# Optimization experiments

Measured on AMD Instinct MI355X. Metric: run time of the kernel, lower is better.

Reference implementation:

```python
import jax, jax.numpy as jnp
import numpy as np

N_MIN = 5
N_MAX = 16
VARIANTS_PER_N = 16
NUM_HIDDEN = 2
HIDDEN = 512
TOTAL_MODELS = (N_MAX - N_MIN + 1) * VARIANTS_PER_N  # 192
BATCH = 65536


def setup_inputs() -> dict:
    key = jax.random.key(0)
    ks = jax.random.split(key, 8)
    n = 16
    s_in = 1.0 / np.sqrt(n)
    s_h = 1.0 / np.sqrt(HIDDEN)
    return {
        "T": jax.random.normal(ks[0], (BATCH, n), dtype=jnp.float32),
        "n": n,
        "variant_index": 3,
        "w_in": jax.random.normal(ks[1], (TOTAL_MODELS, HIDDEN, N_MAX), dtype=jnp.float32) * s_in,
        "b_in": jax.random.normal(ks[2], (TOTAL_MODELS, HIDDEN), dtype=jnp.float32) * 0.01,
        "w_hid": jax.random.normal(ks[3], (TOTAL_MODELS, NUM_HIDDEN, HIDDEN, HIDDEN), dtype=jnp.float32) * s_h,
        "b_hid": jax.random.normal(ks[4], (TOTAL_MODELS, NUM_HIDDEN, HIDDEN), dtype=jnp.float32) * 0.01,
        "w_out": jax.random.normal(ks[5], (TOTAL_MODELS, N_MAX + 1, HIDDEN), dtype=jnp.float32) * s_h,
        "b_out": jax.random.normal(ks[6], (TOTAL_MODELS, N_MAX + 1), dtype=jnp.float32) * 0.01,
    }


def _distortion(X, n):
    # X: (B, n+1). Z[:, n-1-i] = sum_j X[:, j] * X[:, j+i+1] (zero-padded shift).
    # lag k = i+1 -> column n-k; loop is over fixed small n (<=16), unrolls statically.
    cols = [jnp.sum(X[:, :-k] * X[:, k:], axis=1) for k in range(1, n + 1)]
    return jnp.stack(cols[::-1], axis=1)  # (B, n)


def reference(T, n, variant_index, w_in, b_in, w_hid, b_hid, w_out, b_out):
    model_idx = (n - N_MIN) * VARIANTS_PER_N + variant_index
    wi = w_in[model_idx]    # (H, N_MAX)
    bi = b_in[model_idx]    # (H,)
    wh = w_hid[model_idx]   # (2, H, H)
    bh = b_hid[model_idx]   # (2, H)
    wo = w_out[model_idx]   # (N_MAX+1, H)
    bo = b_out[model_idx]   # (N_MAX+1,)

    T_pad = jnp.pad(T, ((0, 0), (0, N_MAX - n)))  # (B, N_MAX)
    norm = jnp.sqrt(jnp.clip(jnp.sum(T_pad * T_pad, axis=1, keepdims=True), 1e-12))
    T_unit = T_pad / norm
    scale = jnp.sqrt(norm)

    x = jax.nn.silu(T_unit @ wi.T + bi)
    for h in range(NUM_HIDDEN):
        x = jax.nn.relu(x @ wh[h].T + bh[h])
    x_full = (x @ wo.T + bo) * scale  # (B, N_MAX+1)

    X_hat = x_full[:, :n + 1]
    X_hat_clamped = jnp.clip(X_hat, -2.0, 2.0)
    error = jnp.mean((_distortion(X_hat, n) - T) ** 2)
    error_clamped = jnp.mean((_distortion(X_hat_clamped, n) - T) ** 2)
    return (X_hat, error, X_hat_clamped, error_clamped)
```

## Files before the change

kernel.cpp:

```cpp
#include <hip/hip_runtime.h>

#define BATCH 65536
#define MT 128
#define NBLK (BATCH / MT)

typedef unsigned short u16;
typedef __bf16 bf16x8 __attribute__((ext_vector_type(8)));
typedef float f32x4 __attribute__((ext_vector_type(4)));

#define WI_OFF 0
#define WH_OFF 16384
#define WO_OFF 540672
#define WS_USH 557056
#define BI_F 0
#define BH_F 512
#define BO_F 1536
#define PART_F 1568
#define PREP_WH 65536
#define PREP_WI 2048
#define PREP_WO 2048
#define PREP_SC 1568
#define PREP_TOTAL (PREP_WH + PREP_WI + PREP_WO + PREP_SC)

__device__ inline u16 f2bf(float f) {
  union { float f; unsigned u; } v; v.f = f;
  unsigned u = v.u + 0x7fffu + ((v.u >> 16) & 1u);
  return (u16)(u >> 16);
}

__global__ void prep_kernel(const float* __restrict__ w_in, const float* __restrict__ b_in,
                            const float* __restrict__ w_hid, const float* __restrict__ b_hid,
                            const float* __restrict__ w_out, const float* __restrict__ b_out,
                            const int* __restrict__ variant, int n,
                            u16* __restrict__ wsu, float* __restrict__ wsf)
{
  const int model = (n - 5) * 16 + variant[0];
  const int i = blockIdx.x * 256 + threadIdx.x;
  if (i < PREP_WH) {
    int g = i & 3, col = (i >> 2) & 511, K32 = (i >> 11) & 15, l = i >> 15;
    const float* src = w_hid + (size_t)model * 524288 + (size_t)l * 262144 + col * 512 + K32 * 32 + g * 8;
    u16* dst = wsu + WH_OFF + (size_t)i * 8;
    #pragma unroll
    for (int e = 0; e < 8; ++e) dst[e] = f2bf(src[e]);
  } else if (i < PREP_WH + PREP_WI) {
    int j = i - PREP_WH;
    int g = j & 3, col = j >> 2;
    u16* dst = wsu + WI_OFF + (size_t)j * 8;
    #pragma unroll
    for (int e = 0; e < 8; ++e) {
      int k = g * 8 + e;
      dst[e] = (k < 16) ? f2bf(w_in[(size_t)model * 8192 + col * 16 + k]) : (u16)0;
    }
  } else if (i < PREP_WH + PREP_WI + PREP_WO) {
    int j = i - PREP_WH - PREP_WI;
    int g = j & 3, col = (j >> 2) & 31, K32 = j >> 7;
    u16* dst = wsu + WO_OFF + (size_t)j * 8;
    #pragma unroll
    for (int e = 0; e < 8; ++e) {
      int k = K32 * 32 + g * 8 + e;
      dst[e] = (col < 17) ? f2bf(w_out[(size_t)model * 8704 + col * 512 + k]) : (u16)0;
    }
  } else if (i < PREP_TOTAL) {
    int j = i - PREP_WH - PREP_WI - PREP_WO;
    if (j < 512)       wsf[BI_F + j] = b_in[(size_t)model * 512 + j];
    else if (j < 1536) wsf[BH_F + (j - 512)] = b_hid[(size_t)model * 1024 + (j - 512)];
    else               { int o = j - 1536; wsf[BO_F + o] = (o < 17) ? b_out[(size_t)model * 17 + o] : 0.f; }
  }
}

__device__ __forceinline__ bf16x8 rdA(const char* xb, int row, int kbyte) {
  return *reinterpret_cast<const bf16x8*>(xb + row * 1024 + (kbyte ^ ((row & 15) << 4)));
}
__device__ __forceinline__ void st16(char* xb, int row, int col, u16 v) {
  *(u16*)(xb + row * 1024 + ((col * 2) ^ ((row & 15) << 4))) = v;
}

template<int NK>
__device__ __forceinline__ void dense_layer(const u16* __restrict__ Wp,
                                            const float* __restrict__ bias, int act,
                                            char* xb, int l15, int q, int c0, int koff)
{
  f32x4 acc[2][4][4];
  #pragma unroll
  for (int p = 0; p < 2; ++p)
    #pragma unroll
    for (int a = 0; a < 4; ++a)
      #pragma unroll
      for (int b = 0; b < 4; ++b) { f32x4 z = {0.f, 0.f, 0.f, 0.f}; acc[p][a][b] = z; }

  const u16* Wl = Wp + (c0 + l15) * 32 + q * 8;

  if constexpr (NK == 1) {
    uint4 b0[4];
    #pragma unroll
    for (int ct = 0; ct < 4; ++ct)
      b0[ct] = *reinterpret_cast<const uint4*>(Wl + ct * 512);
    const int kb = q * 16;
    #pragma unroll
    for (int p = 0; p < 2; ++p)
      #pragma unroll
      for (int mt = 0; mt < 4; ++mt) {
        bf16x8 a = rdA(xb, p * 64 + mt * 16 + l15, kb);
        #pragma unroll
        for (int ct = 0; ct < 4; ++ct)
          acc[p][mt][ct] = __builtin_amdgcn_mfma_f32_16x16x32_bf16(
              a, __builtin_bit_cast(bf16x8, b0[ct]), acc[p][mt][ct], 0, 0, 0);
      }
  } else {
    uint4 bc[4], bn[4];
    {
      const u16* p = Wl + (size_t)koff * 16384;
      #pragma unroll
      for (int ct = 0; ct < 4; ++ct)
        bc[ct] = *reinterpret_cast<const uint4*>(p + ct * 512);
    }
    #pragma unroll 1
    for (int i = 0; i < NK; i += 2) {
      {
        const int Kb = (i + 1) ^ koff;
        const u16* p = Wl + (size_t)Kb * 16384;
        #pragma unroll
        for (int ct = 0; ct < 4; ++ct)
          bn[ct] = *reinterpret_cast<const uint4*>(p + ct * 512);
      }
      {
        const int kb = ((i ^ koff) * 64) + q * 16;
        #pragma unroll
        for (int p = 0; p < 2; ++p)
          #pragma unroll
          for (int mt = 0; mt < 4; ++mt) {
            bf16x8 a = rdA(xb, p * 64 + mt * 16 + l15, kb);
            #pragma unroll
            for (int ct = 0; ct < 4; ++ct)
              acc[p][mt][ct] = __builtin_amdgcn_mfma_f32_16x16x32_bf16(
                  a, __builtin_bit_cast(bf16x8, bc[ct]), acc[p][mt][ct], 0, 0, 0);
          }
      }
      {
        const int Kc = ((i + 2) & (NK - 1)) ^ koff;
        const u16* p = Wl + (size_t)Kc * 16384;
        #pragma unroll
        for (int ct = 0; ct < 4; ++ct)
          bc[ct] = *reinterpret_cast<const uint4*>(p + ct * 512);
      }
      {
        const int kb = (((i + 1) ^ koff) * 64) + q * 16;
        #pragma unroll
        for (int p = 0; p < 2; ++p)
          #pragma unroll
          for (int mt = 0; mt < 4; ++mt) {
            bf16x8 a = rdA(xb, p * 64 + mt * 16 + l15, kb);
            #pragma unroll
            for (int ct = 0; ct < 4; ++ct)
              acc[p][mt][ct] = __builtin_amdgcn_mfma_f32_16x16x32_bf16(
                  a, __builtin_bit_cast(bf16x8, bn[ct]), acc[p][mt][ct], 0, 0, 0);
          }
      }
    }
  }
  __syncthreads();

  float bv[4];
  #pragma unroll
  for (int ct = 0; ct < 4; ++ct) bv[ct] = bias[c0 + ct * 16 + l15];
  #pragma unroll
  for (int p = 0; p < 2; ++p)
    #pragma unroll
    for (int mt = 0; mt < 4; ++mt)
      #pragma unroll
      for (int ct = 0; ct < 4; ++ct)
        #pragma unroll
        for (int j = 0; j < 4; ++j) {
          int row = p * 64 + mt * 16 + q * 4 + j;
          float z = acc[p][mt][ct][j] + bv[ct];
          float h = act ? fmaxf(z, 0.f) : z / (1.f + __expf(-z));
          st16(xb, row, c0 + ct * 16 + l15, f2bf(h));
        }
  __syncthreads();
}

template<int CN>
__global__ __launch_bounds__(512, 2) void fused_kernel(
    const float* __restrict__ T, const u16* __restrict__ wsu,
    const float* __restrict__ wsf, float* __restrict__ Xout, float* __restrict__ Xcout,
    float* __restrict__ errPart, int n_arg)
{
  const int n = CN ? CN : n_arg;
  __shared__ u16 xs[MT * 512];
  __shared__ float xo[MT * 20];
  __shared__ float scaleS[MT];
  __shared__ float ered[8][2];

  const int tid = threadIdx.x;
  const int blk = blockIdx.x;
  const int lane = tid & 63;
  const int wid = tid >> 6;
  const int l15 = lane & 15;
  const int q = lane >> 4;
  const int c0 = wid * 64;
  const int koff = (blk >> 3) & 15;
  char* xb = (char*)xs;

  {
    const int r = tid >> 2, j = tid & 3;
    const size_t gr = (size_t)blk * MT + r;
    const float* tp = T + gr * n;
    float v[4]; float ss = 0.f;
    #pragma unroll
    for (int c = 0; c < 4; ++c) {
      int k = j * 4 + c;
      v[c] = (k < n) ? tp[k] : 0.f;
      ss += v[c] * v[c];
    }
    ss += __shfl_xor(ss, 1); ss += __shfl_xor(ss, 2);
    float norm = sqrtf(ss < 1e-12f ? 1e-12f : ss);
    float rn = 1.f / norm;
    if (j == 0) scaleS[r] = sqrtf(norm);
    #pragma unroll
    for (int c = 0; c < 4; ++c) {
      st16(xb, r, j * 4 + c, f2bf(v[c] * rn));
      st16(xb, r, 16 + j * 4 + c, 0);
    }
  }
  __syncthreads();

  dense_layer<1 >(wsu + WI_OFF,          wsf + BI_F,       0, xb, l15, q, c0, 0);
  dense_layer<16>(wsu + WH_OFF,          wsf + BH_F,       1, xb, l15, q, c0, koff);
  dense_layer<16>(wsu + WH_OFF + 262144, wsf + BH_F + 512, 1, xb, l15, q, c0, koff);

  {
    f32x4 oacc[2];
    { f32x4 z = {0.f, 0.f, 0.f, 0.f}; oacc[0] = z; oacc[1] = z; }
    const int bofs2 = l15 * 32 + q * 8;
    uint4 ob[2], on[2];
    #pragma unroll
    for (int ct = 0; ct < 2; ++ct)
      ob[ct] = *reinterpret_cast<const uint4*>(wsu + WO_OFF + bofs2 + ct * 512);
    #pragma unroll
    for (int K2 = 0; K2 < 16; K2 += 2) {
      #pragma unroll
      for (int ct = 0; ct < 2; ++ct)
        on[ct] = *reinterpret_cast<const uint4*>(wsu + WO_OFF + (K2 + 1) * 1024 + bofs2 + ct * 512);
      {
        bf16x8 a = rdA(xb, wid * 16 + l15, K2 * 64 + q * 16);
        #pragma unroll
        for (int ct = 0; ct < 2; ++ct)
          oacc[ct] = __builtin_amdgcn_mfma_f32_16x16x32_bf16(
              a, __builtin_bit_cast(bf16x8, ob[ct]), oacc[ct], 0, 0, 0);
      }
      if (K2 + 2 < 16) {
        #pragma unroll
        for (int ct = 0; ct < 2; ++ct)
          ob[ct] = *reinterpret_cast<const uint4*>(wsu + WO_OFF + (K2 + 2) * 1024 + bofs2 + ct * 512);
      }
      {
        bf16x8 a = rdA(xb, wid * 16 + l15, (K2 + 1) * 64 + q * 16);
        #pragma unroll
        for (int ct = 0; ct < 2; ++ct)
          oacc[ct] = __builtin_amdgcn_mfma_f32_16x16x32_bf16(
              a, __builtin_bit_cast(bf16x8, on[ct]), oacc[ct], 0, 0, 0);
      }
    }
    #pragma unroll
    for (int ct = 0; ct < 2; ++ct)
      #pragma unroll
      for (int j = 0; j < 4; ++j) {
        int o = ct * 16 + l15;
        int row = wid * 16 + q * 4 + j;
        if (o <= n) {
          float val = (oacc[ct][j] + wsf[BO_F + o]) * scaleS[row];
          size_t gr = (size_t)blk * MT + row;
          float cv = fminf(fmaxf(val, -2.f), 2.f);
          Xout[gr * (n + 1) + o] = val;
          Xcout[gr * (n + 1) + o] = cv;
          xo[row * 20 + o] = val;
        }
      }
  }
  __syncthreads();

  {
    const int r = tid >> 2, j = tid & 3;
    const size_t gr = (size_t)blk * MT + r;
    float x[17], cx[17];
    #pragma unroll
    for (int i = 0; i < 17; ++i) {
      float v = (i <= n) ? xo[r * 20 + i] : 0.f;
      x[i] = v; cx[i] = fminf(fmaxf(v, -2.f), 2.f);
    }
    float e = 0.f, ec = 0.f;
    #pragma unroll
    for (int kk = 0; kk < 4; ++kk) {
      int k = j + 1 + kk * 4;
      if (k <= n) {
        float d = 0.f, dc = 0.f;
        #pragma unroll
        for (int i = 0; i < 16; ++i) {
          if (i + k <= 16) {
            if (i + k <= n) { d += x[i] * x[i + k]; dc += cx[i] * cx[i + k]; }
          }
        }
        float tvv = T[gr * n + (n - k)];
        float r1 = d - tvv, r2 = dc - tvv;
        e += r1 * r1; ec += r2 * r2;
      }
    }
    e += __shfl_xor(e, 1);  ec += __shfl_xor(ec, 1);
    e += __shfl_xor(e, 2);  ec += __shfl_xor(ec, 2);
    e += __shfl_xor(e, 4);  ec += __shfl_xor(ec, 4);
    e += __shfl_xor(e, 8);  ec += __shfl_xor(ec, 8);
    e += __shfl_xor(e, 16); ec += __shfl_xor(ec, 16);
    e += __shfl_xor(e, 32); ec += __shfl_xor(ec, 32);
    if (lane == 0) { ered[wid][0] = e; ered[wid][1] = ec; }
  }
  __syncthreads();
  if (tid == 0) {
    float e = 0.f, ec = 0.f;
    #pragma unroll
    for (int w = 0; w < 8; ++w) { e += ered[w][0]; ec += ered[w][1]; }
    errPart[blk * 2]     = e;
    errPart[blk * 2 + 1] = ec;
  }
}

__global__ void finalize_kernel(const float* __restrict__ part, float* __restrict__ e0,
                                float* __restrict__ e1, float inv)
{
  __shared__ float se[4][2];
  const int t = threadIdx.x;
  float e = 0.f, ec = 0.f;
  for (int b = t; b < NBLK; b += 256) { e += part[2 * b]; ec += part[2 * b + 1]; }
  e += __shfl_xor(e, 1);  ec += __shfl_xor(ec, 1);
  e += __shfl_xor(e, 2);  ec += __shfl_xor(ec, 2);
  e += __shfl_xor(e, 4);  ec += __shfl_xor(ec, 4);
  e += __shfl_xor(e, 8);  ec += __shfl_xor(ec, 8);
  e += __shfl_xor(e, 16); ec += __shfl_xor(ec, 16);
  e += __shfl_xor(e, 32); ec += __shfl_xor(ec, 32);
  if ((t & 63) == 0) { se[t >> 6][0] = e; se[t >> 6][1] = ec; }
  __syncthreads();
  if (t == 0) {
    float te = 0.f, tec = 0.f;
    #pragma unroll
    for (int w = 0; w < 4; ++w) { te += se[w][0]; tec += se[w][1]; }
    e0[0] = te * inv;
    e1[0] = tec * inv;
  }
}

extern "C" void kernel_launch(void* const* d_in, const int* in_sizes, int n_in,
                              void* d_out, int out_size, void* d_ws, size_t ws_size,
                              hipStream_t stream)
{
  const float* T       = (const float*)d_in[0];
  const int*   variant = (const int*)d_in[2];
  const float* w_in    = (const float*)d_in[3];
  const float* b_in    = (const float*)d_in[4];
  const float* w_hid   = (const float*)d_in[5];
  const float* b_hid   = (const float*)d_in[6];
  const float* w_out   = (const float*)d_in[7];
  const float* b_out   = (const float*)d_in[8];
  const int n = in_sizes[0] / BATCH;

  u16* wsu = (u16*)d_ws;
  float* wsf = (float*)((char*)d_ws + (size_t)WS_USH * 2);
  float* out = (float*)d_out;
  const size_t xe = (size_t)BATCH * (n + 1);
  float* Xo  = out;
  float* eP  = out + xe;
  float* Xc  = out + xe + 1;
  float* ecP = out + 2 * xe + 1;

  const int prepBlocks = (PREP_TOTAL + 255) / 256;
  prep_kernel<<<prepBlocks, 256, 0, stream>>>(w_in, b_in, w_hid, b_hid, w_out, b_out,
                                              variant, n, wsu, wsf);
  if (n == 16)
    fused_kernel<16><<<NBLK, 512, 0, stream>>>(T, wsu, wsf, Xo, Xc, wsf + PART_F, n);
  else
    fused_kernel<0><<<NBLK, 512, 0, stream>>>(T, wsu, wsf, Xo, Xc, wsf + PART_F, n);
  finalize_kernel<<<1, 256, 0, stream>>>(wsf + PART_F, eP, ecP, 1.f / (float)((size_t)BATCH * n));
}
```

Before: 135.6 us.

## Triple-buffer weight loads, prefetch next layer weights, cache T in LDS

Replaces the double-buffered, rolled K loop (which used a per-block koff rotation to stagger weight reads) with a fully unrolled triple-buffered prefetch of weight fragments. The first fragment of each next layer's weights is loaded before the barrier and activation epilogue, so that latency overlaps the epilogue. s_setprio is raised around the MFMA sections, and T is staged in LDS so the error pass does not re-read it from global memory. The cost is more VGPRs under the 512x2 launch bound, a larger unrolled code body, and dropping koff, which may concentrate L2 traffic on the same weight lines across blocks.

Measured after the change: 236.3 us. 74.2% more time.

```diff
diff --git a/kernel.cpp b/kernel.cpp
--- a/kernel.cpp
+++ b/kernel.cpp
@@ -77,8 +77,10 @@
 
 template<int NK>
 __device__ __forceinline__ void dense_layer(const u16* __restrict__ Wp,
+                                            const u16* __restrict__ Wnext,
                                             const float* __restrict__ bias, int act,
-                                            char* xb, int l15, int q, int c0, int koff)
+                                            char* xb, int l15, int q, int c0,
+                                            uint4 (&pre)[4])
 {
   f32x4 acc[2][4][4];
   #pragma unroll
@@ -90,12 +92,25 @@
 
   const u16* Wl = Wp + (c0 + l15) * 32 + q * 8;
 
-  if constexpr (NK == 1) {
-    uint4 b0[4];
+  uint4 buf[3][4];
+  #pragma unroll
+  for (int ct = 0; ct < 4; ++ct) buf[0][ct] = pre[ct];
+  if constexpr (NK > 1) {
     #pragma unroll
     for (int ct = 0; ct < 4; ++ct)
-      b0[ct] = *reinterpret_cast<const uint4*>(Wl + ct * 512);
-    const int kb = q * 16;
+      buf[1][ct] = *reinterpret_cast<const uint4*>(Wl + 16384 + ct * 512);
+  }
+
+  #pragma unroll
+  for (int i = 0; i < NK; ++i) {
+    if (i + 2 < NK) {
+      #pragma unroll
+      for (int ct = 0; ct < 4; ++ct)
+        buf[(i + 2) % 3][ct] =
+            *reinterpret_cast<const uint4*>(Wl + (size_t)(i + 2) * 16384 + ct * 512);
+    }
+    __builtin_amdgcn_s_setprio(1);
+    const int kb = i * 64 + q * 16;
     #pragma unroll
     for (int p = 0; p < 2; ++p)
       #pragma unroll
@@ -104,59 +119,16 @@
         #pragma unroll
         for (int ct = 0; ct < 4; ++ct)
           acc[p][mt][ct] = __builtin_amdgcn_mfma_f32_16x16x32_bf16(
-              a, __builtin_bit_cast(bf16x8, b0[ct]), acc[p][mt][ct], 0, 0, 0);
+              a, __builtin_bit_cast(bf16x8, buf[i % 3][ct]), acc[p][mt][ct], 0, 0, 0);
       }
-  } else {
-    uint4 bc[4], bn[4];
-    {
-      const u16* p = Wl + (size_t)koff * 16384;
-      #pragma unroll
-      for (int ct = 0; ct < 4; ++ct)
-        bc[ct] = *reinterpret_cast<const uint4*>(p + ct * 512);
-    }
-    #pragma unroll 1
-    for (int i = 0; i < NK; i += 2) {
-      {
-        const int Kb = (i + 1) ^ koff;
-        const u16* p = Wl + (size_t)Kb * 16384;
-        #pragma unroll
-        for (int ct = 0; ct < 4; ++ct)
-          bn[ct] = *reinterpret_cast<const uint4*>(p + ct * 512);
-      }
-      {
-        const int kb = ((i ^ koff) * 64) + q * 16;
-        #pragma unroll
-        for (int p = 0; p < 2; ++p)
-          #pragma unroll
-          for (int mt = 0; mt < 4; ++mt) {
-            bf16x8 a = rdA(xb, p * 64 + mt * 16 + l15, kb);
-            #pragma unroll
-            for (int ct = 0; ct < 4; ++ct)
-              acc[p][mt][ct] = __builtin_amdgcn_mfma_f32_16x16x32_bf16(
-                  a, __builtin_bit_cast(bf16x8, bc[ct]), acc[p][mt][ct], 0, 0, 0);
-          }
-      }
-      {
-        const int Kc = ((i + 2) & (NK - 1)) ^ koff;
-        const u16* p = Wl + (size_t)Kc * 16384;
-        #pragma unroll
-        for (int ct = 0; ct < 4; ++ct)
-          bc[ct] = *reinterpret_cast<const uint4*>(p + ct * 512);
-      }
-      {
-        const int kb = (((i + 1) ^ koff) * 64) + q * 16;
-        #pragma unroll
-        for (int p = 0; p < 2; ++p)
-          #pragma unroll
-          for (int mt = 0; mt < 4; ++mt) {
-            bf16x8 a = rdA(xb, p * 64 + mt * 16 + l15, kb);
-            #pragma unroll
-            for (int ct = 0; ct < 4; ++ct)
-              acc[p][mt][ct] = __builtin_amdgcn_mfma_f32_16x16x32_bf16(
-                  a, __builtin_bit_cast(bf16x8, bn[ct]), acc[p][mt][ct], 0, 0, 0);
-          }
-      }
-    }
+    __builtin_amdgcn_s_setprio(0);
+  }
+
+  if (Wnext != nullptr) {
+    const u16* Wn = Wnext + (c0 + l15) * 32 + q * 8;
+    #pragma unroll
+    for (int ct = 0; ct < 4; ++ct)
+      pre[ct] = *reinterpret_cast<const uint4*>(Wn + ct * 512);
   }
   __syncthreads();
 
@@ -188,6 +160,7 @@
   const int n = CN ? CN : n_arg;
   __shared__ u16 xs[MT * 512];
   __shared__ float xo[MT * 20];
+  __shared__ float ts[MT * 16];
   __shared__ float scaleS[MT];
   __shared__ float ered[8][2];
 
@@ -198,8 +171,15 @@
   const int l15 = lane & 15;
   const int q = lane >> 4;
   const int c0 = wid * 64;
-  const int koff = (blk >> 3) & 15;
   char* xb = (char*)xs;
+
+  uint4 pre[4];
+  {
+    const u16* WiL = wsu + WI_OFF + (c0 + l15) * 32 + q * 8;
+    #pragma unroll
+    for (int ct = 0; ct < 4; ++ct)
+      pre[ct] = *reinterpret_cast<const uint4*>(WiL + ct * 512);
+  }
 
   {
     const int r = tid >> 2, j = tid & 3;
@@ -220,46 +200,40 @@
     for (int c = 0; c < 4; ++c) {
       st16(xb, r, j * 4 + c, f2bf(v[c] * rn));
       st16(xb, r, 16 + j * 4 + c, 0);
-    }
-  }
-  __syncthreads();
-
-  dense_layer<1 >(wsu + WI_OFF,          wsf + BI_F,       0, xb, l15, q, c0, 0);
-  dense_layer<16>(wsu + WH_OFF,          wsf + BH_F,       1, xb, l15, q, c0, koff);
-  dense_layer<16>(wsu + WH_OFF + 262144, wsf + BH_F + 512, 1, xb, l15, q, c0, koff);
+      ts[r * 16 + j * 4 + c] = v[c];
+    }
+  }
+  __syncthreads();
+
+  dense_layer<1 >(wsu + WI_OFF, wsu + WH_OFF, wsf + BI_F, 0, xb, l15, q, c0, pre);
+  dense_layer<16>(wsu + WH_OFF, wsu + WH_OFF + 262144, wsf + BH_F, 1, xb, l15, q, c0, pre);
+  dense_layer<16>(wsu + WH_OFF + 262144, nullptr, wsf + BH_F + 512, 1, xb, l15, q, c0, pre);
 
   {
     f32x4 oacc[2];
     { f32x4 z = {0.f, 0.f, 0.f, 0.f}; oacc[0] = z; oacc[1] = z; }
     const int bofs2 = l15 * 32 + q * 8;
-    uint4 ob[2], on[2];
-    #pragma unroll
-    for (int ct = 0; ct < 2; ++ct)
-      ob[ct] = *reinterpret_cast<const uint4*>(wsu + WO_OFF + bofs2 + ct * 512);
-    #pragma unroll
-    for (int K2 = 0; K2 < 16; K2 += 2) {
+    uint4 ob[3][2];
+    #pragma unroll
+    for (int s = 0; s < 2; ++s)
       #pragma unroll
       for (int ct = 0; ct < 2; ++ct)
-        on[ct] = *reinterpret_cast<const uint4*>(wsu + WO_OFF + (K2 + 1) * 1024 + bofs2 + ct * 512);
-      {
-        bf16x8 a = rdA(xb, wid * 16 + l15, K2 * 64 + q * 16);
+        ob[s][ct] = *reinterpret_cast<const uint4*>(wsu + WO_OFF + s * 1024 + bofs2 + ct * 512);
+    #pragma unroll
+    for (int K = 0; K < 16; ++K) {
+      if (K + 2 < 16) {
         #pragma unroll
         for (int ct = 0; ct < 2; ++ct)
-          oacc[ct] = __builtin_amdgcn_mfma_f32_16x16x32_bf16(
-              a, __builtin_bit_cast(bf16x8, ob[ct]), oacc[ct], 0, 0, 0);
+          ob[(K + 2) % 3][ct] =
+              *reinterpret_cast<const uint4*>(wsu + WO_OFF + (K + 2) * 1024 + bofs2 + ct * 512);
       }
-      if (K2 + 2 < 16) {
-        #pragma unroll
-        for (int ct = 0; ct < 2; ++ct)
-          ob[ct] = *reinterpret_cast<const uint4*>(wsu + WO_OFF + (K2 + 2) * 1024 + bofs2 + ct * 512);
-      }
-      {
-        bf16x8 a = rdA(xb, wid * 16 + l15, (K2 + 1) * 64 + q * 16);
-        #pragma unroll
-        for (int ct = 0; ct < 2; ++ct)
-          oacc[ct] = __builtin_amdgcn_mfma_f32_16x16x32_bf16(
-              a, __builtin_bit_cast(bf16x8, on[ct]), oacc[ct], 0, 0, 0);
-      }
+      __builtin_amdgcn_s_setprio(1);
+      bf16x8 a = rdA(xb, wid * 16 + l15, K * 64 + q * 16);
+      #pragma unroll
+      for (int ct = 0; ct < 2; ++ct)
+        oacc[ct] = __builtin_amdgcn_mfma_f32_16x16x32_bf16(
+            a, __builtin_bit_cast(bf16x8, ob[K % 3][ct]), oacc[ct], 0, 0, 0);
+      __builtin_amdgcn_s_setprio(0);
     }
     #pragma unroll
     for (int ct = 0; ct < 2; ++ct)
@@ -281,7 +255,6 @@
 
   {
     const int r = tid >> 2, j = tid & 3;
-    const size_t gr = (size_t)blk * MT + r;
     float x[17], cx[17];
     #pragma unroll
     for (int i = 0; i < 17; ++i) {
@@ -300,7 +273,7 @@
             if (i + k <= n) { d += x[i] * x[i + k]; dc += cx[i] * cx[i + k]; }
           }
         }
-        float tvv = T[gr * n + (n - k)];
+        float tvv = ts[r * 16 + (n - k)];
         float r1 = d - tvv, r2 = dc - tvv;
         e += r1 * r1; ec += r2 * r2;
       }
```

## Retile dense layers to 2x4 warp grid and cache T in shared memory

Applied to the files above, without the earlier changes.

The dense layers now split the 128x512 output tile into a 2x4 grid of warps, each owning 64 rows by 128 columns, instead of each warp covering all 128 rows for 64 columns. Each warp therefore does half as many LDS activation reads per MFMA but loads twice as many weight fragments into registers. The per-block K-offset rotation used to spread weight reads across blocks is dropped. The input T is also kept in shared memory so the distortion-error stage no longer re-reads it from global memory, and the output-layer loop is no longer unrolled. Register pressure rises because the accumulators and double-buffered B fragments double in size.

After: 152.3 us. 12.3% more time.

```diff
diff --git a/kernel.cpp b/kernel.cpp
--- a/kernel.cpp
+++ b/kernel.cpp
@@ -78,104 +78,89 @@
 template<int NK>
 __device__ __forceinline__ void dense_layer(const u16* __restrict__ Wp,
                                             const float* __restrict__ bias, int act,
-                                            char* xb, int l15, int q, int c0, int koff)
-{
-  f32x4 acc[2][4][4];
+                                            char* xb, int l15, int q, int r0, int c0)
+{
+  f32x4 acc[4][8];
   #pragma unroll
-  for (int p = 0; p < 2; ++p)
-    #pragma unroll
-    for (int a = 0; a < 4; ++a)
-      #pragma unroll
-      for (int b = 0; b < 4; ++b) { f32x4 z = {0.f, 0.f, 0.f, 0.f}; acc[p][a][b] = z; }
+  for (int a = 0; a < 4; ++a)
+    #pragma unroll
+    for (int b = 0; b < 8; ++b) { f32x4 z = {0.f, 0.f, 0.f, 0.f}; acc[a][b] = z; }
 
   const u16* Wl = Wp + (c0 + l15) * 32 + q * 8;
 
   if constexpr (NK == 1) {
-    uint4 b0[4];
-    #pragma unroll
-    for (int ct = 0; ct < 4; ++ct)
+    uint4 b0[8];
+    #pragma unroll
+    for (int ct = 0; ct < 8; ++ct)
       b0[ct] = *reinterpret_cast<const uint4*>(Wl + ct * 512);
     const int kb = q * 16;
     #pragma unroll
-    for (int p = 0; p < 2; ++p)
-      #pragma unroll
-      for (int mt = 0; mt < 4; ++mt) {
-        bf16x8 a = rdA(xb, p * 64 + mt * 16 + l15, kb);
-        #pragma unroll
-        for (int ct = 0; ct < 4; ++ct)
-          acc[p][mt][ct] = __builtin_amdgcn_mfma_f32_16x16x32_bf16(
-              a, __builtin_bit_cast(bf16x8, b0[ct]), acc[p][mt][ct], 0, 0, 0);
-      }
+    for (int mt = 0; mt < 4; ++mt) {
+      bf16x8 a = rdA(xb, r0 + mt * 16 + l15, kb);
+      #pragma unroll
+      for (int ct = 0; ct < 8; ++ct)
+        acc[mt][ct] = __builtin_amdgcn_mfma_f32_16x16x32_bf16(
+            a, __builtin_bit_cast(bf16x8, b0[ct]), acc[mt][ct], 0, 0, 0);
+    }
   } else {
-    uint4 bc[4], bn[4];
-    {
-      const u16* p = Wl + (size_t)koff * 16384;
-      #pragma unroll
-      for (int ct = 0; ct < 4; ++ct)
-        bc[ct] = *reinterpret_cast<const uint4*>(p + ct * 512);
-    }
+    uint4 bc[8], bn[8];
+    #pragma unroll
+    for (int ct = 0; ct < 8; ++ct)
+      bc[ct] = *reinterpret_cast<const uint4*>(Wl + ct * 512);
     #pragma unroll 1
     for (int i = 0; i < NK; i += 2) {
       {
-        const int Kb = (i + 1) ^ koff;
-        const u16* p = Wl + (size_t)Kb * 16384;
-        #pragma unroll
-        for (int ct = 0; ct < 4; ++ct)
+        const u16* p = Wl + (size_t)(i + 1) * 16384;
+        #pragma unroll
+        for (int ct = 0; ct < 8; ++ct)
           bn[ct] = *reinterpret_cast<const uint4*>(p + ct * 512);
       }
       {
-        const int kb = ((i ^ koff) * 64) + q * 16;
-        #pragma unroll
-        for (int p = 0; p < 2; ++p)
+        const int kb = i * 64 + q * 16;
+        #pragma unroll
+        for (int mt = 0; mt < 4; ++mt) {
+          bf16x8 a = rdA(xb, r0 + mt * 16 + l15, kb);
           #pragma unroll
-          for (int mt = 0; mt < 4; ++mt) {
-            bf16x8 a = rdA(xb, p * 64 + mt * 16 + l15, kb);
-            #pragma unroll
-            for (int ct = 0; ct < 4; ++ct)
-              acc[p][mt][ct] = __builtin_amdgcn_mfma_f32_16x16x32_bf16(
-                  a, __builtin_bit_cast(bf16x8, bc[ct]), acc[p][mt][ct], 0, 0, 0);
-          }
-      }
-      {
-        const int Kc = ((i + 2) & (NK - 1)) ^ koff;
-        const u16* p = Wl + (size_t)Kc * 16384;
-        #pragma unroll
-        for (int ct = 0; ct < 4; ++ct)
+          for (int ct = 0; ct < 8; ++ct)
+            acc[mt][ct] = __builtin_amdgcn_mfma_f32_16x16x32_bf16(
+                a, __builtin_bit_cast(bf16x8, bc[ct]), acc[mt][ct], 0, 0, 0);
+        }
+      }
+      {
+        const u16* p = Wl + (size_t)((i + 2) & (NK - 1)) * 16384;
+        #pragma unroll
+        for (int ct = 0; ct < 8; ++ct)
           bc[ct] = *reinterpret_cast<const uint4*>(p + ct * 512);
       }
       {
-        const int kb = (((i + 1) ^ koff) * 64) + q * 16;
-        #pragma unroll
-        for (int p = 0; p < 2; ++p)
+        const int kb = (i + 1) * 64 + q * 16;
+        #pragma unroll
+        for (int mt = 0; mt < 4; ++mt) {
+          bf16x8 a = rdA(xb, r0 + mt * 16 + l15, kb);
           #pragma unroll
-          for (int mt = 0; mt < 4; ++mt) {
-            bf16x8 a = rdA(xb, p * 64 + mt * 16 + l15, kb);
-            #pragma unroll
-            for (int ct = 0; ct < 4; ++ct)
-              acc[p][mt][ct] = __builtin_amdgcn_mfma_f32_16x16x32_bf16(
-                  a, __builtin_bit_cast(bf16x8, bn[ct]), acc[p][mt][ct], 0, 0, 0);
-          }
-      }
-    }
-  }
-  __syncthreads();
-
-  float bv[4];
+          for (int ct = 0; ct < 8; ++ct)
+            acc[mt][ct] = __builtin_amdgcn_mfma_f32_16x16x32_bf16(
+                a, __builtin_bit_cast(bf16x8, bn[ct]), acc[mt][ct], 0, 0, 0);
+        }
+      }
+    }
+  }
+  __syncthreads();
+
+  float bv[8];
   #pragma unroll
-  for (int ct = 0; ct < 4; ++ct) bv[ct] = bias[c0 + ct * 16 + l15];
+  for (int ct = 0; ct < 8; ++ct) bv[ct] = bias[c0 + ct * 16 + l15];
   #pragma unroll
-  for (int p = 0; p < 2; ++p)
-    #pragma unroll
-    for (int mt = 0; mt < 4; ++mt)
-      #pragma unroll
-      for (int ct = 0; ct < 4; ++ct)
-        #pragma unroll
-        for (int j = 0; j < 4; ++j) {
-          int row = p * 64 + mt * 16 + q * 4 + j;
-          float z = acc[p][mt][ct][j] + bv[ct];
-          float h = act ? fmaxf(z, 0.f) : z / (1.f + __expf(-z));
-          st16(xb, row, c0 + ct * 16 + l15, f2bf(h));
-        }
+  for (int mt = 0; mt < 4; ++mt)
+    #pragma unroll
+    for (int ct = 0; ct < 8; ++ct)
+      #pragma unroll
+      for (int j = 0; j < 4; ++j) {
+        int row = r0 + mt * 16 + q * 4 + j;
+        float z = acc[mt][ct][j] + bv[ct];
+        float h = act ? fmaxf(z, 0.f) : z / (1.f + __expf(-z));
+        st16(xb, row, c0 + ct * 16 + l15, f2bf(h));
+      }
   __syncthreads();
 }
 
@@ -188,6 +173,7 @@
   const int n = CN ? CN : n_arg;
   __shared__ u16 xs[MT * 512];
   __shared__ float xo[MT * 20];
+  __shared__ float ts[MT * 16];
   __shared__ float scaleS[MT];
   __shared__ float ered[8][2];
 
@@ -197,8 +183,8 @@
   const int wid = tid >> 6;
   const int l15 = lane & 15;
   const int q = lane >> 4;
-  const int c0 = wid * 64;
-  const int koff = (blk >> 3) & 15;
+  const int r0 = (wid >> 2) * 64;
+  const int c0 = (wid & 3) * 128;
   char* xb = (char*)xs;
 
   {
@@ -220,13 +206,14 @@
     for (int c = 0; c < 4; ++c) {
       st16(xb, r, j * 4 + c, f2bf(v[c] * rn));
       st16(xb, r, 16 + j * 4 + c, 0);
-    }
-  }
-  __syncthreads();
-
-  dense_layer<1 >(wsu + WI_OFF,          wsf + BI_F,       0, xb, l15, q, c0, 0);
-  dense_layer<16>(wsu + WH_OFF,          wsf + BH_F,       1, xb, l15, q, c0, koff);
-  dense_layer<16>(wsu + WH_OFF + 262144, wsf + BH_F + 512, 1, xb, l15, q, c0, koff);
+      ts[r * 16 + j * 4 + c] = v[c];
+    }
+  }
+  __syncthreads();
+
+  dense_layer<1 >(wsu + WI_OFF,          wsf + BI_F,       0, xb, l15, q, r0, c0);
+  dense_layer<16>(wsu + WH_OFF,          wsf + BH_F,       1, xb, l15, q, r0, c0);
+  dense_layer<16>(wsu + WH_OFF + 262144, wsf + BH_F + 512, 1, xb, l15, q, r0, c0);
 
   {
     f32x4 oacc[2];
@@ -236,11 +223,11 @@
     #pragma unroll
     for (int ct = 0; ct < 2; ++ct)
       ob[ct] = *reinterpret_cast<const uint4*>(wsu + WO_OFF + bofs2 + ct * 512);
-    #pragma unroll
+    #pragma unroll 1
     for (int K2 = 0; K2 < 16; K2 += 2) {
       #pragma unroll
       for (int ct = 0; ct < 2; ++ct)
-        on[ct] = *reinterpret_cast<const uint4*>(wsu + WO_OFF + (K2 + 1) * 1024 + bofs2 + ct * 512);
+        on[ct] = *reinterpret_cast<const uint4*>(wsu + WO_OFF + (size_t)(K2 + 1) * 1024 + bofs2 + ct * 512);
       {
         bf16x8 a = rdA(xb, wid * 16 + l15, K2 * 64 + q * 16);
         #pragma unroll
@@ -248,11 +235,9 @@
           oacc[ct] = __builtin_amdgcn_mfma_f32_16x16x32_bf16(
               a, __builtin_bit_cast(bf16x8, ob[ct]), oacc[ct], 0, 0, 0);
       }
-      if (K2 + 2 < 16) {
-        #pragma unroll
-        for (int ct = 0; ct < 2; ++ct)
-          ob[ct] = *reinterpret_cast<const uint4*>(wsu + WO_OFF + (K2 + 2) * 1024 + bofs2 + ct * 512);
-      }
+      #pragma unroll
+      for (int ct = 0; ct < 2; ++ct)
+        ob[ct] = *reinterpret_cast<const uint4*>(wsu + WO_OFF + (size_t)((K2 + 2) & 15) * 1024 + bofs2 + ct * 512);
       {
         bf16x8 a = rdA(xb, wid * 16 + l15, (K2 + 1) * 64 + q * 16);
         #pragma unroll
@@ -281,7 +266,6 @@
 
   {
     const int r = tid >> 2, j = tid & 3;
-    const size_t gr = (size_t)blk * MT + r;
     float x[17], cx[17];
     #pragma unroll
     for (int i = 0; i < 17; ++i) {
@@ -300,7 +284,7 @@
             if (i + k <= n) { d += x[i] * x[i + k]; dc += cx[i] * cx[i + k]; }
           }
         }
-        float tvv = T[gr * n + (n - k)];
+        float tvv = ts[r * 16 + (n - k)];
         float r1 = d - tvv, r2 = dc - tvv;
         e += r1 * r1; ec += r2 * r2;
       }
```
